# Optimization experiments

Measured on AMD Instinct MI355X. Metric: run time of the kernel, lower is better.

## Reference

```python
import jax, jax.numpy as jnp
import numpy as np

D_MODEL = 768
NHEAD = 12
D_K = D_MODEL // NHEAD
D_FF = 3072
EPS = 1e-6


def layer_norm(x, a, b):
    # torch LayerNorm here: mean/std over last dim, std is UNBIASED (n-1), eps added to std
    n = x.shape[-1]
    m = jnp.mean(x, axis=-1, keepdims=True)
    var = jnp.sum((x - m) ** 2, axis=-1, keepdims=True) / (n - 1)
    return a * (x - m) / (jnp.sqrt(var) + EPS) + b


def setup_inputs() -> dict:
    key = jax.random.key(0)
    ks = jax.random.split(key, 12)
    B, S = 2, 2048
    s = 1.0 / np.sqrt(D_MODEL)
    inp = {
        'x': jax.random.normal(ks[0], (B, S, D_MODEL), jnp.float32),
        'mask': jnp.ones((B, 1, S), jnp.int32),
        'Wq': jax.random.normal(ks[1], (D_MODEL, D_MODEL), jnp.float32) * s,
        'bq': jnp.zeros((D_MODEL,), jnp.float32),
        'Wk': jax.random.normal(ks[2], (D_MODEL, D_MODEL), jnp.float32) * s,
        'bk': jnp.zeros((D_MODEL,), jnp.float32),
        'Wv': jax.random.normal(ks[3], (D_MODEL, D_MODEL), jnp.float32) * s,
        'bv': jnp.zeros((D_MODEL,), jnp.float32),
        'Wo': jax.random.normal(ks[4], (D_MODEL, D_MODEL), jnp.float32) * s,
        'bo': jnp.zeros((D_MODEL,), jnp.float32),
        'ln1_a': jnp.ones((D_MODEL,), jnp.float32),
        'ln1_b': jnp.zeros((D_MODEL,), jnp.float32),
        'W1': jax.random.normal(ks[5], (D_MODEL, D_FF), jnp.float32) * s,
        'b1': jnp.zeros((D_FF,), jnp.float32),
        'W2': jax.random.normal(ks[6], (D_FF, D_MODEL), jnp.float32) * (1.0 / np.sqrt(D_FF)),
        'b2': jnp.zeros((D_MODEL,), jnp.float32),
        'ln2_a': jnp.ones((D_MODEL,), jnp.float32),
        'ln2_b': jnp.zeros((D_MODEL,), jnp.float32),
    }
    return inp


def reference(x, mask, Wq, bq, Wk, bk, Wv, bv, Wo, bo, ln1_a, ln1_b, W1, b1, W2, b2, ln2_a, ln2_b):
    B, S, _ = x.shape
    # --- sublayer 1: pre-norm self-attention + residual (dropout = eval/no-op) ---
    h = layer_norm(x, ln1_a, ln1_b)
    q = (h @ Wq + bq).reshape(B, S, NHEAD, D_K).transpose(0, 2, 1, 3)  # [B,H,S,Dk]
    k = (h @ Wk + bk).reshape(B, S, NHEAD, D_K).transpose(0, 2, 1, 3)
    v = (h @ Wv + bv).reshape(B, S, NHEAD, D_K).transpose(0, 2, 1, 3)
    scores = jnp.einsum('bhqd,bhkd->bhqk', q, k) / np.sqrt(D_K)  # [B,H,S,S]
    scores = jnp.where(mask[:, None] == 0, jnp.float32(-1e9), scores)
    attn = jax.nn.softmax(scores, axis=-1)
    ctx = jnp.einsum('bhqk,bhkd->bhqd', attn, v)  # [B,H,S,Dk]
    ctx = ctx.transpose(0, 2, 1, 3).reshape(B, S, D_MODEL)
    x = x + (ctx @ Wo + bo)
    # --- sublayer 2: pre-norm FFN + residual ---
    h2 = layer_norm(x, ln2_a, ln2_b)
    ff = jax.nn.relu(h2 @ W1 + b1) @ W2 + b2
    return x + ff
```

## Files before the change

### kernel.cpp

```cpp
#include <hip/hip_runtime.h>
#include <hip/hip_bf16.h>
#include <stdint.h>

#define DM 768
#define DFF 3072
#define NH 12
#define DK 64
#define SS 2048
#define NTOK 4096
#define KCH 4

typedef __hip_bfloat16 bf16;
typedef short bf16x8 __attribute__((ext_vector_type(8)));
typedef float f32x4 __attribute__((ext_vector_type(4)));

#define MFMA16(a, b, c) __builtin_amdgcn_mfma_f32_16x16x32_bf16((a), (b), (c), 0, 0, 0)

#define QSCALE 0.18033688011112042f

static __device__ __forceinline__ bf16 f2b(float f) { return __float2bfloat16(f); }
static __device__ __forceinline__ unsigned short f2b_bits(float f) {
    bf16 h = __float2bfloat16(f);
    return *reinterpret_cast<unsigned short*>(&h);
}
static __device__ __forceinline__ float b2f(bf16 h) { return __bfloat162float(h); }

static __device__ __forceinline__ void g2l16(const void* g, void* l) {
    __builtin_amdgcn_global_load_lds(
        (const __attribute__((address_space(1))) unsigned int*)g,
        (__attribute__((address_space(3))) unsigned int*)(uintptr_t)l,
        16, 0, 0);
}

__global__ __launch_bounds__(256) void transpose_cvt(const float* __restrict__ W,
                                                     bf16* __restrict__ WT,
                                                     int K, int N) {
    __shared__ float tile[32][33];
    int n0 = blockIdx.x * 32, k0 = blockIdx.y * 32;
    int tx = threadIdx.x & 31, ty = threadIdx.x >> 5;
#pragma unroll
    for (int r = ty; r < 32; r += 8)
        tile[r][tx] = W[(size_t)(k0 + r) * N + n0 + tx];
    __syncthreads();
#pragma unroll
    for (int r = ty; r < 32; r += 8)
        WT[(size_t)(n0 + r) * K + k0 + tx] = f2b(tile[tx][r]);
}

__global__ __launch_bounds__(256) void transpose_cvt4(const float* W0, const float* W1,
                                                      const float* W2, const float* W3,
                                                      bf16* T0, bf16* T1, bf16* T2, bf16* T3) {
    __shared__ float tile[32][33];
    const float* W = (blockIdx.z == 0) ? W0 : (blockIdx.z == 1) ? W1 : (blockIdx.z == 2) ? W2 : W3;
    bf16* WT = (blockIdx.z == 0) ? T0 : (blockIdx.z == 1) ? T1 : (blockIdx.z == 2) ? T2 : T3;
    int n0 = blockIdx.x * 32, k0 = blockIdx.y * 32;
    int tx = threadIdx.x & 31, ty = threadIdx.x >> 5;
#pragma unroll
    for (int r = ty; r < 32; r += 8)
        tile[r][tx] = W[(size_t)(k0 + r) * DM + n0 + tx];
    __syncthreads();
#pragma unroll
    for (int r = ty; r < 32; r += 8)
        WT[(size_t)(n0 + r) * DM + k0 + tx] = f2b(tile[tx][r]);
}

__global__ __launch_bounds__(256) void ln_fwd(const float* __restrict__ x,
                                              const float* __restrict__ g,
                                              const float* __restrict__ be,
                                              bf16* __restrict__ out) {
    int wid = threadIdx.x >> 6, lane = threadIdx.x & 63;
    int row = blockIdx.x * 4 + wid;
    const float* xr = x + (size_t)row * DM;
    float v[12];
    float s = 0.f;
#pragma unroll
    for (int i = 0; i < 12; ++i) { v[i] = xr[lane + i * 64]; s += v[i]; }
#pragma unroll
    for (int off = 32; off >= 1; off >>= 1) s += __shfl_xor(s, off);
    float mean = s * (1.f / 768.f);
    float s2 = 0.f;
#pragma unroll
    for (int i = 0; i < 12; ++i) { float d = v[i] - mean; s2 += d * d; }
#pragma unroll
    for (int off = 32; off >= 1; off >>= 1) s2 += __shfl_xor(s2, off);
    float rstd = 1.f / (sqrtf(s2 * (1.f / 767.f)) + 1e-6f);
    bf16* orow = out + (size_t)row * DM;
#pragma unroll
    for (int i = 0; i < 12; ++i) {
        int c = lane + i * 64;
        orow[c] = f2b(g[c] * (v[i] - mean) * rstd + be[c]);
    }
}

__device__ __forceinline__ void gemm_core(const bf16* __restrict__ A,
                                          const bf16* __restrict__ BT,
                                          int K, int bm, int bn,
                                          bf16* As, bf16* Bs,
                                          f32x4 acc[4][4]) {
    int tid = threadIdx.x;
    int lane = tid & 63, quad = lane >> 4, lid = lane & 15;
    int wid = tid >> 6;
    int wm = (wid >> 1) * 64, wn = (wid & 1) * 64;
    int s0 = tid, s1 = tid + 256;
    int r0 = s0 >> 2, c0 = (s0 & 3) ^ ((r0 >> 1) & 3);
    int r1 = s1 >> 2, c1 = (s1 & 3) ^ ((r1 >> 1) & 3);
    const bf16* A0 = A + (size_t)(bm + r0) * K + c0 * 8;
    const bf16* A1 = A + (size_t)(bm + r1) * K + c1 * 8;
    const bf16* B0 = BT + (size_t)(bn + r0) * K + c0 * 8;
    const bf16* B1 = BT + (size_t)(bn + r1) * K + c1 * 8;
    int rdc = quad ^ ((lid >> 1) & 3);
    g2l16(A0, As + s0 * 8);
    g2l16(B0, Bs + s0 * 8);
    g2l16(A1, As + s1 * 8);
    g2l16(B1, Bs + s1 * 8);
    for (int k0 = 0; k0 < K; k0 += 32) {
        __syncthreads();
        int cur = (k0 >> 5) & 1;
        if (k0 + 32 < K) {
            int nb = (cur ^ 1) * 4096;
            g2l16(A0 + k0 + 32, As + nb + s0 * 8);
            g2l16(B0 + k0 + 32, Bs + nb + s0 * 8);
            g2l16(A1 + k0 + 32, As + nb + s1 * 8);
            g2l16(B1 + k0 + 32, Bs + nb + s1 * 8);
        }
        const bf16* Ac = As + cur * 4096;
        const bf16* Bc = Bs + cur * 4096;
        bf16x8 af[4], bfr[4];
#pragma unroll
        for (int i = 0; i < 4; ++i) af[i]  = *(const bf16x8*)&Ac[(wm + i * 16 + lid) * 32 + rdc * 8];
#pragma unroll
        for (int j = 0; j < 4; ++j) bfr[j] = *(const bf16x8*)&Bc[(wn + j * 16 + lid) * 32 + rdc * 8];
#pragma unroll
        for (int i = 0; i < 4; ++i)
#pragma unroll
            for (int j = 0; j < 4; ++j)
                acc[i][j] = MFMA16(af[i], bfr[j], acc[i][j]);
    }
}

__global__ __launch_bounds__(256) void gemm_qkv(const bf16* __restrict__ A,
                                                const bf16* __restrict__ WqT,
                                                const bf16* __restrict__ WkT,
                                                const bf16* __restrict__ WvT,
                                                const float* __restrict__ bq,
                                                const float* __restrict__ bk,
                                                const float* __restrict__ bv,
                                                bf16* __restrict__ qb,
                                                bf16* __restrict__ kb,
                                                bf16* __restrict__ vtb) {
    __shared__ bf16 As[2 * 128 * 32];
    __shared__ bf16 Bs[2 * 128 * 32];
    int which = blockIdx.x / 6;
    int bn = (blockIdx.x % 6) * 128;
    int bm = blockIdx.y * 128;
    const bf16* BT = (which == 0) ? WqT : (which == 1) ? WkT : WvT;
    const float* bias = (which == 0) ? bq : (which == 1) ? bk : bv;
    f32x4 acc[4][4] = {};
    gemm_core(A, BT, DM, bm, bn, As, Bs, acc);

    int tid = threadIdx.x, wid = tid >> 6, lane = tid & 63, quad = lane >> 4, lid = lane & 15;
    int wm = (wid >> 1) * 64, wn = (wid & 1) * 64;
    float sc = (which == 0) ? QSCALE : 1.f;
#pragma unroll
    for (int j = 0; j < 4; ++j) {
        int col = bn + wn + j * 16 + lid;
        float bb = bias[col];
        int hh = col >> 6, d = col & 63;
#pragma unroll
        for (int i = 0; i < 4; ++i) {
            int rowbase = bm + wm + i * 16 + quad * 4;
            int b = rowbase >> 11;
            int s0 = rowbase & 2047;
            if (which == 2) {
                ushort4 pk;
                pk.x = f2b_bits(acc[i][j][0] + bb);
                pk.y = f2b_bits(acc[i][j][1] + bb);
                pk.z = f2b_bits(acc[i][j][2] + bb);
                pk.w = f2b_bits(acc[i][j][3] + bb);
                *(ushort4*)&vtb[(((size_t)b * NH + hh) * DK + d) * SS + s0] = pk;
            } else {
                bf16* dst = which ? kb : qb;
#pragma unroll
                for (int r = 0; r < 4; ++r)
                    dst[(((size_t)b * NH + hh) * SS + (s0 + r)) * DK + d] = f2b((acc[i][j][r] + bb) * sc);
            }
        }
    }
}

template <int EPI>
__global__ __launch_bounds__(256) void gemm_ep(const bf16* __restrict__ A,
                                               const bf16* __restrict__ BT,
                                               const float* __restrict__ bias,
                                               const float* __restrict__ res,
                                               void* __restrict__ outp,
                                               int N, int K) {
    __shared__ bf16 As[2 * 128 * 32];
    __shared__ bf16 Bs[2 * 128 * 32];
    int bm = blockIdx.y * 128, bn = blockIdx.x * 128;
    f32x4 acc[4][4] = {};
    gemm_core(A, BT, K, bm, bn, As, Bs, acc);

    int tid = threadIdx.x, wid = tid >> 6, lane = tid & 63, quad = lane >> 4, lid = lane & 15;
    int wm = (wid >> 1) * 64, wn = (wid & 1) * 64;
#pragma unroll
    for (int j = 0; j < 4; ++j) {
        int col = bn + wn + j * 16 + lid;
        float bb = bias[col];
#pragma unroll
        for (int i = 0; i < 4; ++i) {
#pragma unroll
            for (int r = 0; r < 4; ++r) {
                int row = bm + wm + i * 16 + quad * 4 + r;
                float v = acc[i][j][r] + bb;
                if (EPI == 2) {
                    ((float*)outp)[(size_t)row * N + col] = res[(size_t)row * N + col] + v;
                } else {
                    ((bf16*)outp)[(size_t)row * N + col] = f2b(fmaxf(v, 0.f));
                }
            }
        }
    }
}

template <int EPI>
__global__ __launch_bounds__(256) void gemm_ep64(const bf16* __restrict__ A,
                                                 const bf16* __restrict__ BT,
                                                 const float* __restrict__ bias,
                                                 const float* __restrict__ res,
                                                 void* __restrict__ outp,
                                                 int N, int K) {
    __shared__ bf16 As[2 * 64 * 32];
    __shared__ bf16 Bs[2 * 128 * 32];
    int bm = blockIdx.y * 64, bn = blockIdx.x * 128;
    int tid = threadIdx.x, wid = tid >> 6, lane = tid & 63, quad = lane >> 4, lid = lane & 15;
    int wm = (wid >> 1) * 32, wn = (wid & 1) * 64;
    f32x4 acc[2][4] = {};
    int ra = tid >> 2, ca = (tid & 3) ^ ((ra >> 1) & 3);
    int s0 = tid, s1 = tid + 256;
    int rb0 = s0 >> 2, cb0 = (s0 & 3) ^ ((rb0 >> 1) & 3);
    int rb1 = s1 >> 2, cb1 = (s1 & 3) ^ ((rb1 >> 1) & 3);
    const bf16* Ap = A + (size_t)(bm + ra) * K + ca * 8;
    const bf16* B0 = BT + (size_t)(bn + rb0) * K + cb0 * 8;
    const bf16* B1 = BT + (size_t)(bn + rb1) * K + cb1 * 8;
    int rdc = quad ^ ((lid >> 1) & 3);
    g2l16(Ap, As + tid * 8);
    g2l16(B0, Bs + s0 * 8);
    g2l16(B1, Bs + s1 * 8);
    for (int k0 = 0; k0 < K; k0 += 32) {
        __syncthreads();
        int cur = (k0 >> 5) & 1;
        if (k0 + 32 < K) {
            g2l16(Ap + k0 + 32, As + (cur ^ 1) * 2048 + tid * 8);
            g2l16(B0 + k0 + 32, Bs + (cur ^ 1) * 4096 + s0 * 8);
            g2l16(B1 + k0 + 32, Bs + (cur ^ 1) * 4096 + s1 * 8);
        }
        const bf16* Ac = As + cur * 2048;
        const bf16* Bc = Bs + cur * 4096;
        bf16x8 af[2], bfr[4];
#pragma unroll
        for (int i = 0; i < 2; ++i) af[i]  = *(const bf16x8*)&Ac[(wm + i * 16 + lid) * 32 + rdc * 8];
#pragma unroll
        for (int j = 0; j < 4; ++j) bfr[j] = *(const bf16x8*)&Bc[(wn + j * 16 + lid) * 32 + rdc * 8];
#pragma unroll
        for (int i = 0; i < 2; ++i)
#pragma unroll
            for (int j = 0; j < 4; ++j)
                acc[i][j] = MFMA16(af[i], bfr[j], acc[i][j]);
    }
#pragma unroll
    for (int j = 0; j < 4; ++j) {
        int col = bn + wn + j * 16 + lid;
        float bb = bias[col];
#pragma unroll
        for (int i = 0; i < 2; ++i) {
#pragma unroll
            for (int r = 0; r < 4; ++r) {
                int row = bm + wm + i * 16 + quad * 4 + r;
                float v = acc[i][j][r] + bb;
                if (EPI == 2) {
                    ((float*)outp)[(size_t)row * N + col] = res[(size_t)row * N + col] + v;
                } else {
                    ((bf16*)outp)[(size_t)row * N + col] = f2b(fmaxf(v, 0.f));
                }
            }
        }
    }
}

__global__ __launch_bounds__(256) void attn_part(const bf16* __restrict__ qb,
                                                 const bf16* __restrict__ kb,
                                                 const bf16* __restrict__ vtb,
                                                 const int* __restrict__ mask,
                                                 bf16* __restrict__ part,
                                                 float* __restrict__ lws) {
    __shared__ bf16 Ks[64 * 64];
    __shared__ bf16 VTs[64 * 64];
    __shared__ bf16 Ps[64 * 72];
    int bh = blockIdx.y;
    int b = bh / NH, h = bh % NH;
    int q0 = blockIdx.x * 64;
    int kc = blockIdx.z;
    const bf16* Q  = qb  + (size_t)bh * SS * DK;
    const bf16* Kp = kb  + (size_t)bh * SS * DK;
    const bf16* VT = vtb + (size_t)bh * DK * SS;
    int tid = threadIdx.x, wid = tid >> 6, lane = tid & 63, quad = lane >> 4, lid = lane & 15;

    int s0 = tid, s1 = tid + 256;
    int r0 = s0 >> 3, c0 = (s0 & 7) ^ (r0 & 7);
    int r1 = s1 >> 3, c1 = (s1 & 7) ^ (r1 & 7);

    const bf16* Qrow = Q + (size_t)(q0 + wid * 16 + lid) * DK;
    bf16x8 qf0 = *(const bf16x8*)&Qrow[quad * 8];
    bf16x8 qf1 = *(const bf16x8*)&Qrow[32 + quad * 8];

    int rdc  = quad ^ (lid & 7);
    int rdc2 = rdc ^ 4;
    const int* mrow = mask + b * SS;

    f32x4 accv[4] = {};
    float l_part[4] = {0.f, 0.f, 0.f, 0.f};

    for (int t = kc * (SS / 64 / KCH); t < (kc + 1) * (SS / 64 / KCH); ++t) {
        int k0 = t * 64;
        __syncthreads();
        g2l16(Kp + (size_t)(k0 + r0) * DK + c0 * 8, Ks + s0 * 8);
        g2l16(Kp + (size_t)(k0 + r1) * DK + c1 * 8, Ks + s1 * 8);
        g2l16(VT + (size_t)r0 * SS + k0 + c0 * 8, VTs + s0 * 8);
        g2l16(VT + (size_t)r1 * SS + k0 + c1 * 8, VTs + s1 * 8);
        __syncthreads();

        int mk[4];
#pragma unroll
        for (int ns = 0; ns < 4; ++ns) mk[ns] = mrow[k0 + ns * 16 + lid];

#pragma unroll
        for (int ns = 0; ns < 4; ++ns) {
            f32x4 sa = {};
            sa = MFMA16(qf0, *(const bf16x8*)&Ks[(ns * 16 + lid) * 64 + rdc * 8], sa);
            sa = MFMA16(qf1, *(const bf16x8*)&Ks[(ns * 16 + lid) * 64 + rdc2 * 8], sa);
#pragma unroll
            for (int r = 0; r < 4; ++r) {
                float pv = mk[ns] ? exp2f(sa[r]) : 0.f;
                Ps[(wid * 16 + quad * 4 + r) * 72 + ns * 16 + lid] = f2b(pv);
                l_part[r] += pv;
            }
        }

#pragma unroll
        for (int ds = 0; ds < 4; ++ds) {
            accv[ds] = MFMA16(*(const bf16x8*)&Ps[(wid * 16 + lid) * 72 + quad * 8],
                              *(const bf16x8*)&VTs[(ds * 16 + lid) * 64 + rdc * 8], accv[ds]);
            accv[ds] = MFMA16(*(const bf16x8*)&Ps[(wid * 16 + lid) * 72 + 32 + quad * 8],
                              *(const bf16x8*)&VTs[(ds * 16 + lid) * 64 + rdc2 * 8], accv[ds]);
        }
    }

#pragma unroll
    for (int r = 0; r < 4; ++r) {
#pragma unroll
        for (int off = 8; off >= 1; off >>= 1) l_part[r] += __shfl_xor(l_part[r], off);
    }
    if (lid == 0) {
#pragma unroll
        for (int r = 0; r < 4; ++r)
            lws[((size_t)kc * (2 * NH) + bh) * SS + q0 + wid * 16 + quad * 4 + r] = l_part[r];
    }

#pragma unroll
    for (int ds = 0; ds < 4; ++ds) {
#pragma unroll
        for (int r = 0; r < 4; ++r) {
            int row = q0 + wid * 16 + quad * 4 + r;
            int col = h * DK + ds * 16 + lid;
            part[((size_t)kc * NTOK + b * SS + row) * DM + col] = f2b(accv[ds][r]);
        }
    }
}

__global__ __launch_bounds__(256) void attn_combine(const bf16* __restrict__ part,
                                                    const float* __restrict__ lws,
                                                    bf16* __restrict__ ctx) {
    int c = blockIdx.x * 256 + threadIdx.x;
    int t = blockIdx.y;
    int h = c >> 6;
    int b = t >> 11, q = t & 2047;
    int bh = b * NH + h;
    float s = 0.f, l = 0.f;
#pragma unroll
    for (int kc = 0; kc < KCH; ++kc) {
        s += b2f(part[((size_t)kc * NTOK + t) * DM + c]);
        l += lws[((size_t)kc * (2 * NH) + bh) * SS + q];
    }
    ctx[(size_t)t * DM + c] = f2b(s / l);
}

extern "C" void kernel_launch(void* const* d_in, const int* in_sizes, int n_in,
                              void* d_out, int out_size, void* d_ws, size_t ws_size,
                              hipStream_t stream) {
    const float* x    = (const float*)d_in[0];
    const int*   mask = (const int*)d_in[1];
    const float* Wq   = (const float*)d_in[2];
    const float* bq   = (const float*)d_in[3];
    const float* Wk   = (const float*)d_in[4];
    const float* bk   = (const float*)d_in[5];
    const float* Wv   = (const float*)d_in[6];
    const float* bv   = (const float*)d_in[7];
    const float* Wo   = (const float*)d_in[8];
    const float* bo   = (const float*)d_in[9];
    const float* ln1a = (const float*)d_in[10];
    const float* ln1b = (const float*)d_in[11];
    const float* W1   = (const float*)d_in[12];
    const float* b1   = (const float*)d_in[13];
    const float* W2   = (const float*)d_in[14];
    const float* b2   = (const float*)d_in[15];
    const float* ln2a = (const float*)d_in[16];
    const float* ln2b = (const float*)d_in[17];
    float* out = (float*)d_out;

    char* w = (char*)d_ws;
    bf16* h   = (bf16*)w; w += (size_t)NTOK * DM * 2;
    bf16* qb  = (bf16*)w; w += (size_t)NTOK * DM * 2;
    bf16* kb  = (bf16*)w; w += (size_t)NTOK * DM * 2;
    bf16* vtb = (bf16*)w; w += (size_t)NTOK * DM * 2;
    bf16* ctx = (bf16*)w; w += (size_t)NTOK * DM * 2;
    bf16* h2  = (bf16*)w; w += (size_t)NTOK * DM * 2;
    bf16* ffa = (bf16*)w; w += (size_t)NTOK * DFF * 2;
    float* x1 = (float*)w; w += (size_t)NTOK * DM * 4;
    bf16* WqT = (bf16*)w; w += (size_t)DM * DM * 2;
    bf16* WkT = (bf16*)w; w += (size_t)DM * DM * 2;
    bf16* WvT = (bf16*)w; w += (size_t)DM * DM * 2;
    bf16* WoT = (bf16*)w; w += (size_t)DM * DM * 2;
    bf16* W1T = (bf16*)w; w += (size_t)DM * DFF * 2;
    bf16* W2T = (bf16*)w; w += (size_t)DM * DFF * 2;

    bf16*  part = ffa;
    float* lws  = x1;

    transpose_cvt4<<<dim3(24, 24, 4), 256, 0, stream>>>(Wq, Wk, Wv, Wo, WqT, WkT, WvT, WoT);
    transpose_cvt<<<dim3(96, 24), 256, 0, stream>>>(W1, W1T, DM, DFF);
    transpose_cvt<<<dim3(24, 96), 256, 0, stream>>>(W2, W2T, DFF, DM);

    ln_fwd<<<NTOK / 4, 256, 0, stream>>>(x, ln1a, ln1b, h);
    gemm_qkv<<<dim3(18, 32), 256, 0, stream>>>(h, WqT, WkT, WvT, bq, bk, bv, qb, kb, vtb);
    attn_part<<<dim3(SS / 64, 2 * NH, KCH), 256, 0, stream>>>(qb, kb, vtb, mask, part, lws);
    attn_combine<<<dim3(DM / 256, NTOK), 256, 0, stream>>>(part, lws, ctx);
    gemm_ep64<2><<<dim3(6, 64), 256, 0, stream>>>(ctx, WoT, bo, x, (void*)x1, DM, DM);
    ln_fwd<<<NTOK / 4, 256, 0, stream>>>(x1, ln2a, ln2b, h2);
    gemm_ep<3><<<dim3(24, 32), 256, 0, stream>>>(h2, W1T, b1, nullptr, (void*)ffa, DFF, DM);
    gemm_ep64<2><<<dim3(6, 64), 256, 0, stream>>>(ffa, W2T, b2, x1, (void*)out, DM, DFF);
}
```

Measured before the change: 310.7 us.

## Load GEMM weight and attention K/V fragments directly from global memory, bypassing LDS

All GEMM kernels now skip staging the weight (B) tile in shared memory. Each wave reads its B fragments straight from global memory into registers, and only the activation tile is double-buffered in LDS. The attention kernel likewise drops K and V^T LDS staging and its two block barriers, loading fragments directly per wave. It also doubles the query tile per block to 128 (two 16-row sub-tiles per wave) so each K/V fragment feeds two MFMAs. This trades LDS traffic and barriers for uncoalesced, latency-exposed global loads that now rely on L2/L1 caching, and it adds register pressure.

```diff
diff --git a/kernel.cpp b/kernel.cpp
--- a/kernel.cpp
+++ b/kernel.cpp
@@ -95,7 +95,7 @@
 __device__ __forceinline__ void gemm_core(const bf16* __restrict__ A,
                                           const bf16* __restrict__ BT,
                                           int K, int bm, int bn,
-                                          bf16* As, bf16* Bs,
+                                          bf16* As,
                                           f32x4 acc[4][4]) {
     int tid = threadIdx.x;
     int lane = tid & 63, quad = lane >> 4, lid = lane & 15;
@@ -106,30 +106,29 @@
     int r1 = s1 >> 2, c1 = (s1 & 3) ^ ((r1 >> 1) & 3);
     const bf16* A0 = A + (size_t)(bm + r0) * K + c0 * 8;
     const bf16* A1 = A + (size_t)(bm + r1) * K + c1 * 8;
-    const bf16* B0 = BT + (size_t)(bn + r0) * K + c0 * 8;
-    const bf16* B1 = BT + (size_t)(bn + r1) * K + c1 * 8;
+    const bf16* Bp0 = BT + (size_t)(bn + wn + 0 * 16 + lid) * K + quad * 8;
+    const bf16* Bp1 = BT + (size_t)(bn + wn + 1 * 16 + lid) * K + quad * 8;
+    const bf16* Bp2 = BT + (size_t)(bn + wn + 2 * 16 + lid) * K + quad * 8;
+    const bf16* Bp3 = BT + (size_t)(bn + wn + 3 * 16 + lid) * K + quad * 8;
     int rdc = quad ^ ((lid >> 1) & 3);
     g2l16(A0, As + s0 * 8);
-    g2l16(B0, Bs + s0 * 8);
     g2l16(A1, As + s1 * 8);
-    g2l16(B1, Bs + s1 * 8);
     for (int k0 = 0; k0 < K; k0 += 32) {
         __syncthreads();
         int cur = (k0 >> 5) & 1;
         if (k0 + 32 < K) {
             int nb = (cur ^ 1) * 4096;
             g2l16(A0 + k0 + 32, As + nb + s0 * 8);
-            g2l16(B0 + k0 + 32, Bs + nb + s0 * 8);
             g2l16(A1 + k0 + 32, As + nb + s1 * 8);
-            g2l16(B1 + k0 + 32, Bs + nb + s1 * 8);
         }
         const bf16* Ac = As + cur * 4096;
-        const bf16* Bc = Bs + cur * 4096;
         bf16x8 af[4], bfr[4];
-#pragma unroll
-        for (int i = 0; i < 4; ++i) af[i]  = *(const bf16x8*)&Ac[(wm + i * 16 + lid) * 32 + rdc * 8];
-#pragma unroll
-        for (int j = 0; j < 4; ++j) bfr[j] = *(const bf16x8*)&Bc[(wn + j * 16 + lid) * 32 + rdc * 8];
+        bfr[0] = *(const bf16x8*)(Bp0 + k0);
+        bfr[1] = *(const bf16x8*)(Bp1 + k0);
+        bfr[2] = *(const bf16x8*)(Bp2 + k0);
+        bfr[3] = *(const bf16x8*)(Bp3 + k0);
+#pragma unroll
+        for (int i = 0; i < 4; ++i) af[i] = *(const bf16x8*)&Ac[(wm + i * 16 + lid) * 32 + rdc * 8];
 #pragma unroll
         for (int i = 0; i < 4; ++i)
 #pragma unroll
@@ -149,14 +148,13 @@
                                                 bf16* __restrict__ kb,
                                                 bf16* __restrict__ vtb) {
     __shared__ bf16 As[2 * 128 * 32];
-    __shared__ bf16 Bs[2 * 128 * 32];
     int which = blockIdx.x / 6;
     int bn = (blockIdx.x % 6) * 128;
     int bm = blockIdx.y * 128;
     const bf16* BT = (which == 0) ? WqT : (which == 1) ? WkT : WvT;
     const float* bias = (which == 0) ? bq : (which == 1) ? bk : bv;
     f32x4 acc[4][4] = {};
-    gemm_core(A, BT, DM, bm, bn, As, Bs, acc);
+    gemm_core(A, BT, DM, bm, bn, As, acc);
 
     int tid = threadIdx.x, wid = tid >> 6, lane = tid & 63, quad = lane >> 4, lid = lane & 15;
     int wm = (wid >> 1) * 64, wn = (wid & 1) * 64;
@@ -196,10 +194,9 @@
                                                void* __restrict__ outp,
                                                int N, int K) {
     __shared__ bf16 As[2 * 128 * 32];
-    __shared__ bf16 Bs[2 * 128 * 32];
     int bm = blockIdx.y * 128, bn = blockIdx.x * 128;
     f32x4 acc[4][4] = {};
-    gemm_core(A, BT, K, bm, bn, As, Bs, acc);
+    gemm_core(A, BT, K, bm, bn, As, acc);
 
     int tid = threadIdx.x, wid = tid >> 6, lane = tid & 63, quad = lane >> 4, lid = lane & 15;
     int wm = (wid >> 1) * 64, wn = (wid & 1) * 64;
@@ -231,37 +228,31 @@
                                                  void* __restrict__ outp,
                                                  int N, int K) {
     __shared__ bf16 As[2 * 64 * 32];
-    __shared__ bf16 Bs[2 * 128 * 32];
     int bm = blockIdx.y * 64, bn = blockIdx.x * 128;
     int tid = threadIdx.x, wid = tid >> 6, lane = tid & 63, quad = lane >> 4, lid = lane & 15;
     int wm = (wid >> 1) * 32, wn = (wid & 1) * 64;
     f32x4 acc[2][4] = {};
     int ra = tid >> 2, ca = (tid & 3) ^ ((ra >> 1) & 3);
-    int s0 = tid, s1 = tid + 256;
-    int rb0 = s0 >> 2, cb0 = (s0 & 3) ^ ((rb0 >> 1) & 3);
-    int rb1 = s1 >> 2, cb1 = (s1 & 3) ^ ((rb1 >> 1) & 3);
     const bf16* Ap = A + (size_t)(bm + ra) * K + ca * 8;
-    const bf16* B0 = BT + (size_t)(bn + rb0) * K + cb0 * 8;
-    const bf16* B1 = BT + (size_t)(bn + rb1) * K + cb1 * 8;
+    const bf16* Bp0 = BT + (size_t)(bn + wn + 0 * 16 + lid) * K + quad * 8;
+    const bf16* Bp1 = BT + (size_t)(bn + wn + 1 * 16 + lid) * K + quad * 8;
+    const bf16* Bp2 = BT + (size_t)(bn + wn + 2 * 16 + lid) * K + quad * 8;
+    const bf16* Bp3 = BT + (size_t)(bn + wn + 3 * 16 + lid) * K + quad * 8;
     int rdc = quad ^ ((lid >> 1) & 3);
     g2l16(Ap, As + tid * 8);
-    g2l16(B0, Bs + s0 * 8);
-    g2l16(B1, Bs + s1 * 8);
     for (int k0 = 0; k0 < K; k0 += 32) {
         __syncthreads();
         int cur = (k0 >> 5) & 1;
-        if (k0 + 32 < K) {
+        if (k0 + 32 < K)
             g2l16(Ap + k0 + 32, As + (cur ^ 1) * 2048 + tid * 8);
-            g2l16(B0 + k0 + 32, Bs + (cur ^ 1) * 4096 + s0 * 8);
-            g2l16(B1 + k0 + 32, Bs + (cur ^ 1) * 4096 + s1 * 8);
-        }
         const bf16* Ac = As + cur * 2048;
-        const bf16* Bc = Bs + cur * 4096;
         bf16x8 af[2], bfr[4];
-#pragma unroll
-        for (int i = 0; i < 2; ++i) af[i]  = *(const bf16x8*)&Ac[(wm + i * 16 + lid) * 32 + rdc * 8];
-#pragma unroll
-        for (int j = 0; j < 4; ++j) bfr[j] = *(const bf16x8*)&Bc[(wn + j * 16 + lid) * 32 + rdc * 8];
+        bfr[0] = *(const bf16x8*)(Bp0 + k0);
+        bfr[1] = *(const bf16x8*)(Bp1 + k0);
+        bfr[2] = *(const bf16x8*)(Bp2 + k0);
+        bfr[3] = *(const bf16x8*)(Bp3 + k0);
+#pragma unroll
+        for (int i = 0; i < 2; ++i) af[i] = *(const bf16x8*)&Ac[(wm + i * 16 + lid) * 32 + rdc * 8];
 #pragma unroll
         for (int i = 0; i < 2; ++i)
 #pragma unroll
@@ -288,92 +279,99 @@
     }
 }
 
-__global__ __launch_bounds__(256) void attn_part(const bf16* __restrict__ qb,
-                                                 const bf16* __restrict__ kb,
-                                                 const bf16* __restrict__ vtb,
-                                                 const int* __restrict__ mask,
-                                                 bf16* __restrict__ part,
-                                                 float* __restrict__ lws) {
-    __shared__ bf16 Ks[64 * 64];
-    __shared__ bf16 VTs[64 * 64];
-    __shared__ bf16 Ps[64 * 72];
+__global__ __launch_bounds__(256, 4) void attn_part(const bf16* __restrict__ qb,
+                                                    const bf16* __restrict__ kb,
+                                                    const bf16* __restrict__ vtb,
+                                                    const int* __restrict__ mask,
+                                                    bf16* __restrict__ part,
+                                                    float* __restrict__ lws) {
+    __shared__ bf16 Ps[128 * 72];
     int bh = blockIdx.y;
     int b = bh / NH, h = bh % NH;
-    int q0 = blockIdx.x * 64;
+    int q0 = blockIdx.x * 128;
     int kc = blockIdx.z;
-    const bf16* Q  = qb  + (size_t)bh * SS * DK;
-    const bf16* Kp = kb  + (size_t)bh * SS * DK;
-    const bf16* VT = vtb + (size_t)bh * DK * SS;
+    const bf16* Kbase = kb  + (size_t)bh * SS * DK;
+    const bf16* Vbase = vtb + (size_t)bh * DK * SS;
     int tid = threadIdx.x, wid = tid >> 6, lane = tid & 63, quad = lane >> 4, lid = lane & 15;
-
-    int s0 = tid, s1 = tid + 256;
-    int r0 = s0 >> 3, c0 = (s0 & 7) ^ (r0 & 7);
-    int r1 = s1 >> 3, c1 = (s1 & 7) ^ (r1 & 7);
-
-    const bf16* Qrow = Q + (size_t)(q0 + wid * 16 + lid) * DK;
-    bf16x8 qf0 = *(const bf16x8*)&Qrow[quad * 8];
-    bf16x8 qf1 = *(const bf16x8*)&Qrow[32 + quad * 8];
-
-    int rdc  = quad ^ (lid & 7);
-    int rdc2 = rdc ^ 4;
+    int wbase = wid * 32;
+
+    bf16x8 qf[2][2];
+#pragma unroll
+    for (int sub = 0; sub < 2; ++sub) {
+        const bf16* Qrow = qb + ((size_t)bh * SS + q0 + wbase + sub * 16 + lid) * DK;
+        qf[sub][0] = *(const bf16x8*)&Qrow[quad * 8];
+        qf[sub][1] = *(const bf16x8*)&Qrow[32 + quad * 8];
+    }
     const int* mrow = mask + b * SS;
 
-    f32x4 accv[4] = {};
-    float l_part[4] = {0.f, 0.f, 0.f, 0.f};
+    f32x4 accv[2][4] = {};
+    float l_part[2][4] = {};
 
     for (int t = kc * (SS / 64 / KCH); t < (kc + 1) * (SS / 64 / KCH); ++t) {
         int k0 = t * 64;
-        __syncthreads();
-        g2l16(Kp + (size_t)(k0 + r0) * DK + c0 * 8, Ks + s0 * 8);
-        g2l16(Kp + (size_t)(k0 + r1) * DK + c1 * 8, Ks + s1 * 8);
-        g2l16(VT + (size_t)r0 * SS + k0 + c0 * 8, VTs + s0 * 8);
-        g2l16(VT + (size_t)r1 * SS + k0 + c1 * 8, VTs + s1 * 8);
-        __syncthreads();
-
-        int mk[4];
-#pragma unroll
-        for (int ns = 0; ns < 4; ++ns) mk[ns] = mrow[k0 + ns * 16 + lid];
-
 #pragma unroll
         for (int ns = 0; ns < 4; ++ns) {
-            f32x4 sa = {};
-            sa = MFMA16(qf0, *(const bf16x8*)&Ks[(ns * 16 + lid) * 64 + rdc * 8], sa);
-            sa = MFMA16(qf1, *(const bf16x8*)&Ks[(ns * 16 + lid) * 64 + rdc2 * 8], sa);
+            const bf16* Krow = Kbase + (size_t)(k0 + ns * 16 + lid) * DK;
+            bf16x8 kf0 = *(const bf16x8*)&Krow[quad * 8];
+            bf16x8 kf1 = *(const bf16x8*)&Krow[32 + quad * 8];
+            int mk = mrow[k0 + ns * 16 + lid];
+#pragma unroll
+            for (int sub = 0; sub < 2; ++sub) {
+                f32x4 sa = {};
+                sa = MFMA16(qf[sub][0], kf0, sa);
+                sa = MFMA16(qf[sub][1], kf1, sa);
+#pragma unroll
+                for (int r = 0; r < 4; ++r) {
+                    float pv = mk ? exp2f(sa[r]) : 0.f;
+                    Ps[(wbase + sub * 16 + quad * 4 + r) * 72 + ns * 16 + lid] = f2b(pv);
+                    l_part[sub][r] += pv;
+                }
+            }
+        }
+        bf16x8 pa[2][2];
+#pragma unroll
+        for (int sub = 0; sub < 2; ++sub) {
+            pa[sub][0] = *(const bf16x8*)&Ps[(wbase + sub * 16 + lid) * 72 + quad * 8];
+            pa[sub][1] = *(const bf16x8*)&Ps[(wbase + sub * 16 + lid) * 72 + 32 + quad * 8];
+        }
+#pragma unroll
+        for (int ds = 0; ds < 4; ++ds) {
+            const bf16* Vrow = Vbase + (size_t)(ds * 16 + lid) * SS + k0;
+            bf16x8 vf0 = *(const bf16x8*)&Vrow[quad * 8];
+            bf16x8 vf1 = *(const bf16x8*)&Vrow[32 + quad * 8];
+#pragma unroll
+            for (int sub = 0; sub < 2; ++sub) {
+                accv[sub][ds] = MFMA16(pa[sub][0], vf0, accv[sub][ds]);
+                accv[sub][ds] = MFMA16(pa[sub][1], vf1, accv[sub][ds]);
+            }
+        }
+    }
+
+#pragma unroll
+    for (int sub = 0; sub < 2; ++sub) {
+#pragma unroll
+        for (int r = 0; r < 4; ++r) {
+#pragma unroll
+            for (int off = 8; off >= 1; off >>= 1)
+                l_part[sub][r] += __shfl_xor(l_part[sub][r], off);
+        }
+        if (lid == 0) {
+#pragma unroll
+            for (int r = 0; r < 4; ++r)
+                lws[((size_t)kc * (2 * NH) + bh) * SS + q0 + wbase + sub * 16 + quad * 4 + r] = l_part[sub][r];
+        }
+    }
+
+#pragma unroll
+    for (int sub = 0; sub < 2; ++sub) {
+#pragma unroll
+        for (int ds = 0; ds < 4; ++ds) {
 #pragma unroll
             for (int r = 0; r < 4; ++r) {
-                float pv = mk[ns] ? exp2f(sa[r]) : 0.f;
-                Ps[(wid * 16 + quad * 4 + r) * 72 + ns * 16 + lid] = f2b(pv);
-                l_part[r] += pv;
-            }
-        }
-
-#pragma unroll
-        for (int ds = 0; ds < 4; ++ds) {
-            accv[ds] = MFMA16(*(const bf16x8*)&Ps[(wid * 16 + lid) * 72 + quad * 8],
-                              *(const bf16x8*)&VTs[(ds * 16 + lid) * 64 + rdc * 8], accv[ds]);
-            accv[ds] = MFMA16(*(const bf16x8*)&Ps[(wid * 16 + lid) * 72 + 32 + quad * 8],
-                              *(const bf16x8*)&VTs[(ds * 16 + lid) * 64 + rdc2 * 8], accv[ds]);
-        }
-    }
-
-#pragma unroll
-    for (int r = 0; r < 4; ++r) {
-#pragma unroll
-        for (int off = 8; off >= 1; off >>= 1) l_part[r] += __shfl_xor(l_part[r], off);
-    }
-    if (lid == 0) {
-#pragma unroll
-        for (int r = 0; r < 4; ++r)
-            lws[((size_t)kc * (2 * NH) + bh) * SS + q0 + wid * 16 + quad * 4 + r] = l_part[r];
-    }
-
-#pragma unroll
-    for (int ds = 0; ds < 4; ++ds) {
-#pragma unroll
-        for (int r = 0; r < 4; ++r) {
-            int row = q0 + wid * 16 + quad * 4 + r;
-            int col = h * DK + ds * 16 + lid;
-            part[((size_t)kc * NTOK + b * SS + row) * DM + col] = f2b(accv[ds][r]);
+                int row = q0 + wbase + sub * 16 + quad * 4 + r;
+                int col = h * DK + ds * 16 + lid;
+                part[((size_t)kc * NTOK + b * SS + row) * DM + col] = f2b(accv[sub][ds][r]);
+            }
         }
     }
 }
@@ -443,7 +441,7 @@
 
     ln_fwd<<<NTOK / 4, 256, 0, stream>>>(x, ln1a, ln1b, h);
     gemm_qkv<<<dim3(18, 32), 256, 0, stream>>>(h, WqT, WkT, WvT, bq, bk, bv, qb, kb, vtb);
-    attn_part<<<dim3(SS / 64, 2 * NH, KCH), 256, 0, stream>>>(qb, kb, vtb, mask, part, lws);
+    attn_part<<<dim3(SS / 128, 2 * NH, KCH), 256, 0, stream>>>(qb, kb, vtb, mask, part, lws);
     attn_combine<<<dim3(DM / 256, NTOK), 256, 0, stream>>>(part, lws, ctx);
     gemm_ep64<2><<<dim3(6, 64), 256, 0, stream>>>(ctx, WoT, bo, x, (void*)x1, DM, DM);
     ln_fwd<<<NTOK / 4, 256, 0, stream>>>(x1, ln2a, ln2b, h2);
```

New measurement: 449.3 us. 44.6% more time.

## Merge weight transposes into one launch and restructure attention P/rowsum via MFMA

Applied to the files above, without the earlier changes.

Folds the three weight-transpose launches into a single flat-grid kernel to cut launch overhead. In attention, QK^T is now computed transposed (K as the A operand), so each lane holds four consecutive keys. This allows vectorised int4 mask loads and packed 8-byte bf16 stores of P into LDS instead of scalar per-element stores. The row-sum of P now comes from an MFMA against a ones vector, replacing per-element accumulation and cross-lane shuffles, at the cost of extra MFMAs and summing the bf16-rounded P values.

```diff
diff --git a/kernel.cpp b/kernel.cpp
--- a/kernel.cpp
+++ b/kernel.cpp
@@ -32,11 +32,26 @@
         16, 0, 0);
 }
 
-__global__ __launch_bounds__(256) void transpose_cvt(const float* __restrict__ W,
-                                                     bf16* __restrict__ WT,
-                                                     int K, int N) {
+__global__ __launch_bounds__(256) void transpose_all(const float* Wq, const float* Wk,
+                                                     const float* Wv, const float* Wo,
+                                                     const float* W1, const float* W2,
+                                                     bf16* WqT, bf16* WkT, bf16* WvT,
+                                                     bf16* WoT, bf16* W1T, bf16* W2T) {
     __shared__ float tile[32][33];
-    int n0 = blockIdx.x * 32, k0 = blockIdx.y * 32;
+    int id = blockIdx.x;
+    const float* W; bf16* WT; int K, N, n0, k0;
+    if (id < 2304) {
+        int z = id / 576, r = id % 576;
+        W  = (z == 0) ? Wq : (z == 1) ? Wk : (z == 2) ? Wv : Wo;
+        WT = (z == 0) ? WqT : (z == 1) ? WkT : (z == 2) ? WvT : WoT;
+        K = 768; N = 768; n0 = (r % 24) * 32; k0 = (r / 24) * 32;
+    } else if (id < 4608) {
+        int r = id - 2304; W = W1; WT = W1T;
+        K = 768; N = 3072; n0 = (r % 96) * 32; k0 = (r / 96) * 32;
+    } else {
+        int r = id - 4608; W = W2; WT = W2T;
+        K = 3072; N = 768; n0 = (r % 24) * 32; k0 = (r / 24) * 32;
+    }
     int tx = threadIdx.x & 31, ty = threadIdx.x >> 5;
 #pragma unroll
     for (int r = ty; r < 32; r += 8)
@@ -45,23 +60,6 @@
 #pragma unroll
     for (int r = ty; r < 32; r += 8)
         WT[(size_t)(n0 + r) * K + k0 + tx] = f2b(tile[tx][r]);
-}
-
-__global__ __launch_bounds__(256) void transpose_cvt4(const float* W0, const float* W1,
-                                                      const float* W2, const float* W3,
-                                                      bf16* T0, bf16* T1, bf16* T2, bf16* T3) {
-    __shared__ float tile[32][33];
-    const float* W = (blockIdx.z == 0) ? W0 : (blockIdx.z == 1) ? W1 : (blockIdx.z == 2) ? W2 : W3;
-    bf16* WT = (blockIdx.z == 0) ? T0 : (blockIdx.z == 1) ? T1 : (blockIdx.z == 2) ? T2 : T3;
-    int n0 = blockIdx.x * 32, k0 = blockIdx.y * 32;
-    int tx = threadIdx.x & 31, ty = threadIdx.x >> 5;
-#pragma unroll
-    for (int r = ty; r < 32; r += 8)
-        tile[r][tx] = W[(size_t)(k0 + r) * DM + n0 + tx];
-    __syncthreads();
-#pragma unroll
-    for (int r = ty; r < 32; r += 8)
-        WT[(size_t)(n0 + r) * DM + k0 + tx] = f2b(tile[tx][r]);
 }
 
 __global__ __launch_bounds__(256) void ln_fwd(const float* __restrict__ x,
@@ -301,7 +299,6 @@
     int b = bh / NH, h = bh % NH;
     int q0 = blockIdx.x * 64;
     int kc = blockIdx.z;
-    const bf16* Q  = qb  + (size_t)bh * SS * DK;
     const bf16* Kp = kb  + (size_t)bh * SS * DK;
     const bf16* VT = vtb + (size_t)bh * DK * SS;
     int tid = threadIdx.x, wid = tid >> 6, lane = tid & 63, quad = lane >> 4, lid = lane & 15;
@@ -310,16 +307,20 @@
     int r0 = s0 >> 3, c0 = (s0 & 7) ^ (r0 & 7);
     int r1 = s1 >> 3, c1 = (s1 & 7) ^ (r1 & 7);
 
-    const bf16* Qrow = Q + (size_t)(q0 + wid * 16 + lid) * DK;
+    const bf16* Qrow = qb + ((size_t)bh * SS + q0 + wid * 16 + lid) * DK;
     bf16x8 qf0 = *(const bf16x8*)&Qrow[quad * 8];
     bf16x8 qf1 = *(const bf16x8*)&Qrow[32 + quad * 8];
+
+    bf16x8 ones;
+#pragma unroll
+    for (int i = 0; i < 8; ++i) ones[i] = (short)0x3F80;
 
     int rdc  = quad ^ (lid & 7);
     int rdc2 = rdc ^ 4;
     const int* mrow = mask + b * SS;
 
     f32x4 accv[4] = {};
-    float l_part[4] = {0.f, 0.f, 0.f, 0.f};
+    f32x4 accl = {};
 
     for (int t = kc * (SS / 64 / KCH); t < (kc + 1) * (SS / 64 / KCH); ++t) {
         int k0 = t * 64;
@@ -330,41 +331,45 @@
         g2l16(VT + (size_t)r1 * SS + k0 + c1 * 8, VTs + s1 * 8);
         __syncthreads();
 
-        int mk[4];
-#pragma unroll
-        for (int ns = 0; ns < 4; ++ns) mk[ns] = mrow[k0 + ns * 16 + lid];
-
 #pragma unroll
         for (int ns = 0; ns < 4; ++ns) {
-            f32x4 sa = {};
-            sa = MFMA16(qf0, *(const bf16x8*)&Ks[(ns * 16 + lid) * 64 + rdc * 8], sa);
-            sa = MFMA16(qf1, *(const bf16x8*)&Ks[(ns * 16 + lid) * 64 + rdc2 * 8], sa);
-#pragma unroll
-            for (int r = 0; r < 4; ++r) {
-                float pv = mk[ns] ? exp2f(sa[r]) : 0.f;
-                Ps[(wid * 16 + quad * 4 + r) * 72 + ns * 16 + lid] = f2b(pv);
-                l_part[r] += pv;
-            }
-        }
+            bf16x8 kf0 = *(const bf16x8*)&Ks[(ns * 16 + lid) * 64 + rdc * 8];
+            bf16x8 kf1 = *(const bf16x8*)&Ks[(ns * 16 + lid) * 64 + rdc2 * 8];
+            f32x4 st = {};
+            st = MFMA16(kf0, qf0, st);
+            st = MFMA16(kf1, qf1, st);
+            int4 mk = *(const int4*)&mrow[k0 + ns * 16 + quad * 4];
+            float p0 = mk.x ? exp2f(st[0]) : 0.f;
+            float p1 = mk.y ? exp2f(st[1]) : 0.f;
+            float p2 = mk.z ? exp2f(st[2]) : 0.f;
+            float p3 = mk.w ? exp2f(st[3]) : 0.f;
+            __hip_bfloat162 h01 = __float22bfloat162_rn(make_float2(p0, p1));
+            __hip_bfloat162 h23 = __float22bfloat162_rn(make_float2(p2, p3));
+            uint2 pw;
+            pw.x = *(unsigned int*)&h01;
+            pw.y = *(unsigned int*)&h23;
+            *(uint2*)&Ps[(wid * 16 + lid) * 72 + ns * 16 + quad * 4] = pw;
+        }
+
+        bf16x8 pa0 = *(const bf16x8*)&Ps[(wid * 16 + lid) * 72 + quad * 8];
+        bf16x8 pa1 = *(const bf16x8*)&Ps[(wid * 16 + lid) * 72 + 32 + quad * 8];
+
+        accl = MFMA16(pa0, ones, accl);
+        accl = MFMA16(pa1, ones, accl);
 
 #pragma unroll
         for (int ds = 0; ds < 4; ++ds) {
-            accv[ds] = MFMA16(*(const bf16x8*)&Ps[(wid * 16 + lid) * 72 + quad * 8],
-                              *(const bf16x8*)&VTs[(ds * 16 + lid) * 64 + rdc * 8], accv[ds]);
-            accv[ds] = MFMA16(*(const bf16x8*)&Ps[(wid * 16 + lid) * 72 + 32 + quad * 8],
-                              *(const bf16x8*)&VTs[(ds * 16 + lid) * 64 + rdc2 * 8], accv[ds]);
-        }
-    }
-
-#pragma unroll
-    for (int r = 0; r < 4; ++r) {
-#pragma unroll
-        for (int off = 8; off >= 1; off >>= 1) l_part[r] += __shfl_xor(l_part[r], off);
-    }
+            bf16x8 vf0 = *(const bf16x8*)&VTs[(ds * 16 + lid) * 64 + rdc * 8];
+            bf16x8 vf1 = *(const bf16x8*)&VTs[(ds * 16 + lid) * 64 + rdc2 * 8];
+            accv[ds] = MFMA16(pa0, vf0, accv[ds]);
+            accv[ds] = MFMA16(pa1, vf1, accv[ds]);
+        }
+    }
+
     if (lid == 0) {
 #pragma unroll
         for (int r = 0; r < 4; ++r)
-            lws[((size_t)kc * (2 * NH) + bh) * SS + q0 + wid * 16 + quad * 4 + r] = l_part[r];
+            lws[((size_t)kc * (2 * NH) + bh) * SS + q0 + wid * 16 + quad * 4 + r] = accl[r];
     }
 
 #pragma unroll
@@ -437,9 +442,8 @@
     bf16*  part = ffa;
     float* lws  = x1;
 
-    transpose_cvt4<<<dim3(24, 24, 4), 256, 0, stream>>>(Wq, Wk, Wv, Wo, WqT, WkT, WvT, WoT);
-    transpose_cvt<<<dim3(96, 24), 256, 0, stream>>>(W1, W1T, DM, DFF);
-    transpose_cvt<<<dim3(24, 96), 256, 0, stream>>>(W2, W2T, DFF, DM);
+    transpose_all<<<6912, 256, 0, stream>>>(Wq, Wk, Wv, Wo, W1, W2,
+                                            WqT, WkT, WvT, WoT, W1T, W2T);
 
     ln_fwd<<<NTOK / 4, 256, 0, stream>>>(x, ln1a, ln1b, h);
     gemm_qkv<<<dim3(18, 32), 256, 0, stream>>>(h, WqT, WkT, WvT, bq, bk, bv, qb, kb, vtb);
```

New measurement: 305.9 us. Within noise of the previous version (-1.6%).
